# Performance work log

Hardware: AMD Instinct MI355X
Metric: run time of the kernel (lower is better)

Reference implementation:

```python
import jax, jax.numpy as jnp
import numpy as np

NEG_SLOPE = 0.2

def gat_layer(x, W, al, ar, src, dst, n_dst):
    # x: [Ns, Fin]; W: [Fin, H*D]; al/ar: [H, D]; src/dst: [E]
    H, D = al.shape
    h = (x @ W).reshape(-1, H, D)          # [Ns, H, D]
    h_dst = h[:n_dst]                       # dst nodes are prefix of src nodes (DGL block)
    el = (h * al).sum(-1)                   # [Ns, H]
    er = (h_dst * ar).sum(-1)               # [Nd, H]
    e = jax.nn.leaky_relu(el[src] + er[dst], NEG_SLOPE)  # [E, H]
    m = jax.ops.segment_max(e, dst, num_segments=n_dst)  # stable edge-softmax
    a = jnp.exp(e - m[dst])
    s = jax.ops.segment_sum(a, dst, num_segments=n_dst)
    alpha = a / s[dst]                      # [E, H]
    msg = h[src] * alpha[:, :, None]        # [E, H, D]
    out = jax.ops.segment_sum(msg, dst, num_segments=n_dst)  # [Nd, H, D]
    return out.reshape(n_dst, H * D)


def setup_inputs() -> dict:
    key = jax.random.key(0)
    ks = jax.random.split(key, 16)
    N0, N1, N2, N3 = 200000, 100000, 50000, 25000
    E0, E1, E2 = 1000000, 500000, 250000
    Fin, Dh, H, C = 256, 64, 3, 40
    inp = {}
    inp['x'] = jax.random.normal(ks[0], (N0, Fin), jnp.float32)
    inp['src0'] = jax.random.randint(ks[1], (E0,), 0, N0, jnp.int32)
    inp['dst0'] = jnp.sort(jax.random.randint(ks[2], (E0,), 0, N1, jnp.int32))
    inp['src1'] = jax.random.randint(ks[3], (E1,), 0, N1, jnp.int32)
    inp['dst1'] = jnp.sort(jax.random.randint(ks[4], (E1,), 0, N2, jnp.int32))
    inp['src2'] = jax.random.randint(ks[5], (E2,), 0, N2, jnp.int32)
    inp['dst2'] = jnp.sort(jax.random.randint(ks[6], (E2,), 0, N3, jnp.int32))
    sc = lambda f: np.float32(1.0 / np.sqrt(f))
    inp['W0'] = jax.random.normal(ks[7], (Fin, H * Dh), jnp.float32) * sc(Fin)
    inp['al0'] = jax.random.normal(ks[8], (H, Dh), jnp.float32) * sc(Dh)
    inp['ar0'] = jax.random.normal(ks[9], (H, Dh), jnp.float32) * sc(Dh)
    inp['W1'] = jax.random.normal(ks[10], (H * Dh, H * Dh), jnp.float32) * sc(H * Dh)
    inp['al1'] = jax.random.normal(ks[11], (H, Dh), jnp.float32) * sc(Dh)
    inp['ar1'] = jax.random.normal(ks[12], (H, Dh), jnp.float32) * sc(Dh)
    inp['W2'] = jax.random.normal(ks[13], (H * Dh, C), jnp.float32) * sc(H * Dh)
    inp['al2'] = jax.random.normal(ks[14], (1, C), jnp.float32) * sc(C)
    inp['ar2'] = jax.random.normal(ks[15], (1, C), jnp.float32) * sc(C)
    return inp


def reference(x, src0, dst0, src1, dst1, src2, dst2,
              W0, al0, ar0, W1, al1, ar1, W2, al2, ar2):
    N1, N2, N3 = 100000, 50000, 25000
    h = gat_layer(x, W0, al0, ar0, src0, dst0, N1)
    h = jax.nn.relu(h)  # dropout is identity in eval/deterministic mode
    h = gat_layer(h, W1, al1, ar1, src1, dst1, N2)
    h = jax.nn.relu(h)
    out = gat_layer(h, W2, al2, ar2, src2, dst2, N3)  # [N3, n_classes]
    return out
```

## Files before the change

kernel.cpp:

```cpp
#include <hip/hip_runtime.h>
#include <math.h>

#define DEV_INLINE __device__ __forceinline__

typedef __attribute__((ext_vector_type(8))) short short8v;
typedef __attribute__((ext_vector_type(4))) float float4v;

DEV_INLINE unsigned short f2bf_rtn(float f) {
  unsigned u = __float_as_uint(f);
  u += 0x7FFFu + ((u >> 16) & 1u);
  return (unsigned short)(u >> 16);
}
DEV_INLINE float bf2f(unsigned short s) { return __uint_as_float(((unsigned)s) << 16); }

DEV_INLINE int soff(int row, int oct) { return row * 32 + ((oct ^ ((row >> 1) & 3)) << 3); }

DEV_INLINE void gload_lds16(const void* g, void* l) {
  __builtin_amdgcn_global_load_lds(
      (const __attribute__((address_space(1))) void*)g,
      (__attribute__((address_space(3))) void*)l, 16, 0, 0);
}

__global__ void prepass_all(const float* __restrict__ W0, const float* __restrict__ W1,
                            const float* __restrict__ W2, short* __restrict__ w0h,
                            short* __restrict__ w0l, short* __restrict__ w1h,
                            short* __restrict__ w1l, short* __restrict__ w2h,
                            short* __restrict__ w2l,
                            const int* __restrict__ d0, const int* __restrict__ d1,
                            const int* __restrict__ d2, int* __restrict__ o0,
                            int* __restrict__ o1, int* __restrict__ o2,
                            int E0, int E1, int E2, int n1, int n2, int n3) {
  const int S0 = 256 * 192, S1 = 192 * 192, S2 = 192 * 48;
  const int WTOT = S0 + S1 + S2;
  int gidx = blockIdx.x * 256 + threadIdx.x;
  if (gidx < WTOT) {
    int idx = gidx;
    const float* W; short *Wh, *Wl; int K; int which;
    if (idx < S0) { W = W0; Wh = w0h; Wl = w0l; K = 256; which = 0; }
    else if (idx < S0 + S1) { idx -= S0; W = W1; Wh = w1h; Wl = w1l; K = 192; which = 1; }
    else { idx -= S0 + S1; W = W2; Wh = w2h; Wl = w2l; K = 192; which = 2; }
    int n = idx / K, k = idx - n * K;
    if (which == 2 && n >= 40) { Wh[idx] = 0; Wl[idx] = 0; return; }
    int N = (which == 2) ? 40 : 192;
    float w = W[(size_t)k * N + n];
    unsigned short h = f2bf_rtn(w);
    Wh[idx] = (short)h;
    Wl[idx] = (short)f2bf_rtn(w - bf2f(h));
    return;
  }
  int i = gidx - WTOT;
  const int* dst; int* off; int E, nd;
  if (i < E0) { dst = d0; off = o0; E = E0; nd = n1; }
  else if (i < E0 + E1) { i -= E0; dst = d1; off = o1; E = E1; nd = n2; }
  else if (i < E0 + E1 + E2) { i -= E0 + E1; dst = d2; off = o2; E = E2; nd = n3; }
  else return;
  int d = dst[i];
  int p = (i == 0) ? -1 : dst[i - 1];
  for (int q = p + 1; q <= d; ++q) off[q] = i;
  if (i == E - 1)
    for (int q = d + 1; q <= nd; ++q) off[q] = E;
}

#define DMA_B(ktv, bufv)                                                      \
  {                                                                           \
    const int kb = (ktv) << 6;                                \
    for (int c = w; c < NT; c += 4) {                                         \
      gload_lds16((const char*)Bth + (size_t)c * (K * 32) + voff + kb,        \
                  (short*)Bs_h[bufv] + c * 512);                              \
      gload_lds16((const char*)Btl + (size_t)c * (K * 32) + voff + kb,        \
                  (short*)Bs_l[bufv] + c * 512);                              \
    }                                                                         \
  }

template <int NT, int H>
__global__ __launch_bounds__(256, 3) void gemm_fused(
    const float* __restrict__ A, const short* __restrict__ Bth,
    const short* __restrict__ Btl, const float* __restrict__ al,
    const float* __restrict__ ar, float* __restrict__ C,
    float* __restrict__ el, float* __restrict__ er,
    int M, int N, int K, int n_dst) {
  constexpr int BN = NT * 16;
  constexpr int TPH = NT / H;
  __shared__ short Bs_h[2][BN * 32], Bs_l[2][BN * 32];
  const int tid = threadIdx.x;
  const int w = tid >> 6, lane = tid & 63;
  const int quad = lane >> 4, l16 = lane & 15;
  const int m0 = blockIdx.x * 64;
  const int arow = m0 + w * 16 + l16;

  const int voff = (lane >> 2) * (K * 2) + ((((lane & 3) ^ ((lane >> 3) & 3))) << 4);

  float4v acc[NT];
#pragma unroll
  for (int nt = 0; nt < NT; ++nt)
#pragma unroll
    for (int r = 0; r < 4; ++r) acc[nt][r] = 0.f;

  const int nk = K >> 5;

  DMA_B(0, 0);
  float4 pa0, pa1;
  if (arow < M) {
    const float* ap = A + (size_t)arow * K + quad * 8;
    pa0 = *(const float4*)ap;
    pa1 = *(const float4*)(ap + 4);
  } else {
    pa0 = make_float4(0.f, 0.f, 0.f, 0.f);
    pa1 = pa0;
  }
  __syncthreads();

  for (int kt = 0; kt < nk; ++kt) {
    const int cur = kt & 1;
    float4 na0, na1;
    if (kt + 1 < nk) {
      if (arow < M) {
        const float* ap = A + (size_t)arow * K + ((kt + 1) << 5) + quad * 8;
        na0 = *(const float4*)ap;
        na1 = *(const float4*)(ap + 4);
      } else {
        na0 = make_float4(0.f, 0.f, 0.f, 0.f);
        na1 = na0;
      }
      DMA_B(kt + 1, cur ^ 1);
    } else {
      na0 = make_float4(0.f, 0.f, 0.f, 0.f);
      na1 = na0;
    }
    short8v afh, afl;
    {
      float vs[8] = {pa0.x, pa0.y, pa0.z, pa0.w, pa1.x, pa1.y, pa1.z, pa1.w};
#pragma unroll
      for (int j = 0; j < 8; ++j) {
        unsigned short hh = f2bf_rtn(vs[j]);
        afh[j] = (short)hh;
        afl[j] = (short)f2bf_rtn(vs[j] - bf2f(hh));
      }
    }
#pragma unroll
    for (int nt = 0; nt < NT; ++nt) {
      int col = nt * 16 + l16;
      short8v bfh = *(const short8v*)(Bs_h[cur] + soff(col, quad));
      short8v bfl = *(const short8v*)(Bs_l[cur] + soff(col, quad));
      acc[nt] = __builtin_amdgcn_mfma_f32_16x16x32_bf16(afh, bfh, acc[nt], 0, 0, 0);
      acc[nt] = __builtin_amdgcn_mfma_f32_16x16x32_bf16(afh, bfl, acc[nt], 0, 0, 0);
      acc[nt] = __builtin_amdgcn_mfma_f32_16x16x32_bf16(afl, bfh, acc[nt], 0, 0, 0);
    }
    if (kt + 1 < nk) __syncthreads();
    pa0 = na0;
    pa1 = na1;
  }

  float av[NT], rv[NT];
#pragma unroll
  for (int nt = 0; nt < NT; ++nt) {
    int col = nt * 16 + l16;
    av[nt] = (col < N) ? al[col] : 0.f;
    rv[nt] = (col < N) ? ar[col] : 0.f;
  }
#pragma unroll
  for (int r = 0; r < 4; ++r) {
    int gm = m0 + w * 16 + quad * 4 + r;
    if (gm >= M) continue;
    float pl[H], pr[H];
#pragma unroll
    for (int h = 0; h < H; ++h) { pl[h] = 0.f; pr[h] = 0.f; }
#pragma unroll
    for (int nt = 0; nt < NT; ++nt) {
      int h = nt / TPH;
      pl[h] = fmaf(acc[nt][r], av[nt], pl[h]);
      pr[h] = fmaf(acc[nt][r], rv[nt], pr[h]);
    }
#pragma unroll
    for (int h = 0; h < H; ++h) {
#pragma unroll
      for (int o = 8; o >= 1; o >>= 1) {
        pl[h] += __shfl_xor(pl[h], o, 16);
        pr[h] += __shfl_xor(pr[h], o, 16);
      }
    }
    if (l16 == 0) {
#pragma unroll
      for (int h = 0; h < H; ++h) {
        el[gm * H + h] = pl[h];
        if (gm < n_dst) er[gm * H + h] = pr[h];
      }
    }
#pragma unroll
    for (int nt = 0; nt < NT; ++nt) {
      int col = nt * 16 + l16;
      if (col < N) C[(size_t)gm * N + col] = acc[nt][r];
    }
  }
}

template <int H, int D, bool RELU>
__global__ __launch_bounds__(256) void agg2_kernel(
    const float* __restrict__ hsrc, const float* __restrict__ el,
    const float* __restrict__ er, const int* __restrict__ src,
    const int* __restrict__ off, float* __restrict__ out, int n_dst) {
  constexpr int F = H * D;
  constexpr int NP = (F + 63) / 64;
  __shared__ float wbuf[16][16][H];
  __shared__ int sbuf[16][16];
  const int g = threadIdx.x >> 4, l = threadIdx.x & 15;
  const int d = blockIdx.x * 16 + g;
  if (d >= n_dst) return;
  const int lo = off[d], hi = off[d + 1];

  if (hi <= lo) {
#pragma unroll
    for (int p = 0; p < NP; ++p) {
      int c4 = (p * 16 + l) * 4;
      if (c4 < F) *(float4*)(out + (size_t)d * F + c4) = make_float4(0.f, 0.f, 0.f, 0.f);
    }
    return;
  }

  float erv[H], s_part[H];
#pragma unroll
  for (int h = 0; h < H; ++h) {
    erv[h] = er[d * H + h];
    s_part[h] = 0.f;
  }
  float4 acc[NP];
#pragma unroll
  for (int p = 0; p < NP; ++p) acc[p] = make_float4(0.f, 0.f, 0.f, 0.f);

  for (int base = lo; base < hi; base += 16) {
    const int i = base + l;
    const bool valid = i < hi;
    const int sid = valid ? src[i] : 0;
#pragma unroll
    for (int h = 0; h < H; ++h) {
      float e = 0.f;
      if (valid) {
        e = el[sid * H + h] + erv[h];
        e = e > 0.f ? e : 0.2f * e;
        e = __expf(e);
      }
      s_part[h] += e;
      wbuf[g][l][h] = e;
    }
    sbuf[g][l] = sid;

    const int cnt = min(16, hi - base);
    float4 hv[NP], hn[NP], hn2[NP];
    {
      int sj = sbuf[g][0];
#pragma unroll
      for (int p = 0; p < NP; ++p) {
        int c4 = (p * 16 + l) * 4;
        hv[p] = (c4 < F) ? *(const float4*)(hsrc + (size_t)sj * F + c4)
                         : make_float4(0.f, 0.f, 0.f, 0.f);
      }
    }
    if (cnt > 1) {
      int sj = sbuf[g][1];
#pragma unroll
      for (int p = 0; p < NP; ++p) {
        int c4 = (p * 16 + l) * 4;
        hn[p] = (c4 < F) ? *(const float4*)(hsrc + (size_t)sj * F + c4)
                         : make_float4(0.f, 0.f, 0.f, 0.f);
      }
    }
    for (int ei = 0; ei < cnt; ++ei) {
      if (ei + 2 < cnt) {
        int sj2 = sbuf[g][ei + 2];
#pragma unroll
        for (int p = 0; p < NP; ++p) {
          int c4 = (p * 16 + l) * 4;
          hn2[p] = (c4 < F) ? *(const float4*)(hsrc + (size_t)sj2 * F + c4)
                            : make_float4(0.f, 0.f, 0.f, 0.f);
        }
      }
#pragma unroll
      for (int p = 0; p < NP; ++p) {
        int c4 = (p * 16 + l) * 4;
        float wc = wbuf[g][ei][c4 / D];
        acc[p].x = fmaf(wc, hv[p].x, acc[p].x);
        acc[p].y = fmaf(wc, hv[p].y, acc[p].y);
        acc[p].z = fmaf(wc, hv[p].z, acc[p].z);
        acc[p].w = fmaf(wc, hv[p].w, acc[p].w);
      }
#pragma unroll
      for (int p = 0; p < NP; ++p) { hv[p] = hn[p]; hn[p] = hn2[p]; }
    }
  }

#pragma unroll
  for (int h = 0; h < H; ++h)
#pragma unroll
    for (int o = 8; o >= 1; o >>= 1) s_part[h] += __shfl_xor(s_part[h], o, 16);

#pragma unroll
  for (int p = 0; p < NP; ++p) {
    int c4 = (p * 16 + l) * 4;
    if (c4 < F) {
      float inv = 1.f / s_part[c4 / D];
      float4 o;
      o.x = acc[p].x * inv; o.y = acc[p].y * inv;
      o.z = acc[p].z * inv; o.w = acc[p].w * inv;
      if (RELU) {
        o.x = fmaxf(o.x, 0.f); o.y = fmaxf(o.y, 0.f);
        o.z = fmaxf(o.z, 0.f); o.w = fmaxf(o.w, 0.f);
      }
      *(float4*)(out + (size_t)d * F + c4) = o;
    }
  }
}

extern "C" void kernel_launch(void* const* d_in, const int* in_sizes, int n_in,
                              void* d_out, int out_size, void* d_ws, size_t ws_size,
                              hipStream_t stream) {
  const float* x   = (const float*)d_in[0];
  const int* src0  = (const int*)d_in[1];
  const int* dst0  = (const int*)d_in[2];
  const int* src1  = (const int*)d_in[3];
  const int* dst1  = (const int*)d_in[4];
  const int* src2  = (const int*)d_in[5];
  const int* dst2  = (const int*)d_in[6];
  const float* W0  = (const float*)d_in[7];
  const float* al0 = (const float*)d_in[8];
  const float* ar0 = (const float*)d_in[9];
  const float* W1  = (const float*)d_in[10];
  const float* al1 = (const float*)d_in[11];
  const float* ar1 = (const float*)d_in[12];
  const float* W2  = (const float*)d_in[13];
  const float* al2 = (const float*)d_in[14];
  const float* ar2 = (const float*)d_in[15];

  const int N0 = 200000, N1 = 100000, N2 = 50000, N3 = 25000;
  const int E0 = in_sizes[1], E1 = in_sizes[3], E2 = in_sizes[5];
  const int Fin = 256, F = 192, C = 40;

  float* ws     = (float*)d_ws;
  float* h_buf  = ws;
  float* o_buf  = h_buf + (size_t)N0 * F;
  float* el_buf = o_buf + (size_t)N1 * F;
  float* er_buf = el_buf + (size_t)N0 * 3;
  short* w0h    = (short*)(er_buf + (size_t)N1 * 3);
  short* w0l    = w0h + 192 * 256;
  short* w1h    = w0l + 192 * 256;
  short* w1l    = w1h + 192 * 192;
  short* w2h    = w1l + 192 * 192;
  short* w2l    = w2h + 48 * 192;
  int*   off0   = (int*)(w2l + 48 * 192);
  int*   off1   = off0 + (N1 + 1);
  int*   off2   = off1 + (N2 + 1);

  dim3 blk(256);

  const int WTOT = 256 * 192 + 192 * 192 + 192 * 48;
  const int ETOT = E0 + E1 + E2;
  prepass_all<<<dim3((WTOT + ETOT + 255) / 256), blk, 0, stream>>>(
      W0, W1, W2, w0h, w0l, w1h, w1l, w2h, w2l,
      dst0, dst1, dst2, off0, off1, off2, E0, E1, E2, N1, N2, N3);

  gemm_fused<12, 3><<<dim3((N0 + 63) / 64), blk, 0, stream>>>(
      x, w0h, w0l, al0, ar0, h_buf, el_buf, er_buf, N0, F, Fin, N1);
  agg2_kernel<3, 64, true><<<dim3((N1 + 15) / 16), blk, 0, stream>>>(
      h_buf, el_buf, er_buf, src0, off0, o_buf, N1);

  gemm_fused<12, 3><<<dim3((N1 + 63) / 64), blk, 0, stream>>>(
      o_buf, w1h, w1l, al1, ar1, h_buf, el_buf, er_buf, N1, F, F, N2);
  agg2_kernel<3, 64, true><<<dim3((N2 + 15) / 16), blk, 0, stream>>>(
      h_buf, el_buf, er_buf, src1, off1, o_buf, N2);

  gemm_fused<3, 1><<<dim3((N2 + 63) / 64), blk, 0, stream>>>(
      o_buf, w2h, w2l, al2, ar2, h_buf, el_buf, er_buf, N2, C, F, N3);
  agg2_kernel<1, 40, false><<<dim3((N3 + 15) / 16), blk, 0, stream>>>(
      h_buf, el_buf, er_buf, src2, off2, (float*)d_out, N3);
}
```

Before: 641.6 us.

## Double GEMM row tile per wave to reuse B fragments and hand-tune waits

```diff
diff --git a/kernel.cpp b/kernel.cpp
--- a/kernel.cpp
+++ b/kernel.cpp
@@ -73,7 +73,7 @@
   }
 
 template <int NT, int H>
-__global__ __launch_bounds__(256, 3) void gemm_fused(
+__global__ __launch_bounds__(256) void gemm_fused(
     const float* __restrict__ A, const short* __restrict__ Bth,
     const short* __restrict__ Btl, const float* __restrict__ al,
     const float* __restrict__ ar, float* __restrict__ C,
@@ -85,56 +85,61 @@
   const int tid = threadIdx.x;
   const int w = tid >> 6, lane = tid & 63;
   const int quad = lane >> 4, l16 = lane & 15;
-  const int m0 = blockIdx.x * 64;
-  const int arow = m0 + w * 16 + l16;
+  const int m0 = blockIdx.x * 128;
 
   const int voff = (lane >> 2) * (K * 2) + ((((lane & 3) ^ ((lane >> 3) & 3))) << 4);
 
-  float4v acc[NT];
-#pragma unroll
-  for (int nt = 0; nt < NT; ++nt)
-#pragma unroll
-    for (int r = 0; r < 4; ++r) acc[nt][r] = 0.f;
+  const int r0 = min(m0 + w * 32 + l16, M - 1);
+  const int r1 = min(m0 + w * 32 + 16 + l16, M - 1);
+  const float* a0p = A + (size_t)r0 * K + quad * 8;
+  const float* a1p = A + (size_t)r1 * K + quad * 8;
+
+  float4v acc[2][NT];
+#pragma unroll
+  for (int mt = 0; mt < 2; ++mt)
+#pragma unroll
+    for (int nt = 0; nt < NT; ++nt)
+#pragma unroll
+      for (int r = 0; r < 4; ++r) acc[mt][nt][r] = 0.f;
 
   const int nk = K >> 5;
 
   DMA_B(0, 0);
-  float4 pa0, pa1;
-  if (arow < M) {
-    const float* ap = A + (size_t)arow * K + quad * 8;
-    pa0 = *(const float4*)ap;
-    pa1 = *(const float4*)(ap + 4);
-  } else {
-    pa0 = make_float4(0.f, 0.f, 0.f, 0.f);
-    pa1 = pa0;
-  }
-  __syncthreads();
+  asm volatile("" ::: "memory");
+  float4 pa00 = *(const float4*)a0p;
+  float4 pa01 = *(const float4*)(a0p + 4);
+  float4 pa10 = *(const float4*)a1p;
+  float4 pa11 = *(const float4*)(a1p + 4);
+  asm volatile("s_waitcnt vmcnt(4)" ::: "memory");
+  asm volatile("s_barrier" ::: "memory");
 
   for (int kt = 0; kt < nk; ++kt) {
     const int cur = kt & 1;
-    float4 na0, na1;
+    float4 na00, na01, na10, na11;
     if (kt + 1 < nk) {
-      if (arow < M) {
-        const float* ap = A + (size_t)arow * K + ((kt + 1) << 5) + quad * 8;
-        na0 = *(const float4*)ap;
-        na1 = *(const float4*)(ap + 4);
-      } else {
-        na0 = make_float4(0.f, 0.f, 0.f, 0.f);
-        na1 = na0;
-      }
       DMA_B(kt + 1, cur ^ 1);
+      asm volatile("" ::: "memory");
+      const int ko = (kt + 1) << 5;
+      na00 = *(const float4*)(a0p + ko);
+      na01 = *(const float4*)(a0p + ko + 4);
+      na10 = *(const float4*)(a1p + ko);
+      na11 = *(const float4*)(a1p + ko + 4);
     } else {
-      na0 = make_float4(0.f, 0.f, 0.f, 0.f);
-      na1 = na0;
-    }
-    short8v afh, afl;
+      na00 = make_float4(0.f, 0.f, 0.f, 0.f);
+      na01 = na00; na10 = na00; na11 = na00;
+    }
+    short8v afh[2], afl[2];
     {
-      float vs[8] = {pa0.x, pa0.y, pa0.z, pa0.w, pa1.x, pa1.y, pa1.z, pa1.w};
+      float vs0[8] = {pa00.x, pa00.y, pa00.z, pa00.w, pa01.x, pa01.y, pa01.z, pa01.w};
+      float vs1[8] = {pa10.x, pa10.y, pa10.z, pa10.w, pa11.x, pa11.y, pa11.z, pa11.w};
 #pragma unroll
       for (int j = 0; j < 8; ++j) {
-        unsigned short hh = f2bf_rtn(vs[j]);
-        afh[j] = (short)hh;
-        afl[j] = (short)f2bf_rtn(vs[j] - bf2f(hh));
+        unsigned short h0 = f2bf_rtn(vs0[j]);
+        afh[0][j] = (short)h0;
+        afl[0][j] = (short)f2bf_rtn(vs0[j] - bf2f(h0));
+        unsigned short h1 = f2bf_rtn(vs1[j]);
+        afh[1][j] = (short)h1;
+        afl[1][j] = (short)f2bf_rtn(vs1[j] - bf2f(h1));
       }
     }
 #pragma unroll
@@ -142,13 +147,19 @@
       int col = nt * 16 + l16;
       short8v bfh = *(const short8v*)(Bs_h[cur] + soff(col, quad));
       short8v bfl = *(const short8v*)(Bs_l[cur] + soff(col, quad));
-      acc[nt] = __builtin_amdgcn_mfma_f32_16x16x32_bf16(afh, bfh, acc[nt], 0, 0, 0);
-      acc[nt] = __builtin_amdgcn_mfma_f32_16x16x32_bf16(afh, bfl, acc[nt], 0, 0, 0);
-      acc[nt] = __builtin_amdgcn_mfma_f32_16x16x32_bf16(afl, bfh, acc[nt], 0, 0, 0);
-    }
-    if (kt + 1 < nk) __syncthreads();
-    pa0 = na0;
-    pa1 = na1;
+#pragma unroll
+      for (int mt = 0; mt < 2; ++mt) {
+        acc[mt][nt] = __builtin_amdgcn_mfma_f32_16x16x32_bf16(afh[mt], bfh, acc[mt][nt], 0, 0, 0);
+        acc[mt][nt] = __builtin_amdgcn_mfma_f32_16x16x32_bf16(afh[mt], bfl, acc[mt][nt], 0, 0, 0);
+        acc[mt][nt] = __builtin_amdgcn_mfma_f32_16x16x32_bf16(afl[mt], bfh, acc[mt][nt], 0, 0, 0);
+      }
+    }
+    if (kt + 1 < nk) {
+      asm volatile("s_waitcnt lgkmcnt(0)" ::: "memory");
+      asm volatile("s_waitcnt vmcnt(4)" ::: "memory");
+      asm volatile("s_barrier" ::: "memory");
+    }
+    pa00 = na00; pa01 = na01; pa10 = na10; pa11 = na11;
   }
 
   float av[NT], rv[NT];
@@ -159,39 +170,41 @@
     rv[nt] = (col < N) ? ar[col] : 0.f;
   }
 #pragma unroll
-  for (int r = 0; r < 4; ++r) {
-    int gm = m0 + w * 16 + quad * 4 + r;
-    if (gm >= M) continue;
-    float pl[H], pr[H];
-#pragma unroll
-    for (int h = 0; h < H; ++h) { pl[h] = 0.f; pr[h] = 0.f; }
-#pragma unroll
-    for (int nt = 0; nt < NT; ++nt) {
-      int h = nt / TPH;
-      pl[h] = fmaf(acc[nt][r], av[nt], pl[h]);
-      pr[h] = fmaf(acc[nt][r], rv[nt], pr[h]);
-    }
-#pragma unroll
-    for (int h = 0; h < H; ++h) {
-#pragma unroll
-      for (int o = 8; o >= 1; o >>= 1) {
-        pl[h] += __shfl_xor(pl[h], o, 16);
-        pr[h] += __shfl_xor(pr[h], o, 16);
-      }
-    }
-    if (l16 == 0) {
+  for (int mt = 0; mt < 2; ++mt)
+#pragma unroll
+    for (int r = 0; r < 4; ++r) {
+      int gm = m0 + w * 32 + mt * 16 + quad * 4 + r;
+      if (gm >= M) continue;
+      float pl[H], pr[H];
+#pragma unroll
+      for (int h = 0; h < H; ++h) { pl[h] = 0.f; pr[h] = 0.f; }
+#pragma unroll
+      for (int nt = 0; nt < NT; ++nt) {
+        int h = nt / TPH;
+        pl[h] = fmaf(acc[mt][nt][r], av[nt], pl[h]);
+        pr[h] = fmaf(acc[mt][nt][r], rv[nt], pr[h]);
+      }
 #pragma unroll
       for (int h = 0; h < H; ++h) {
-        el[gm * H + h] = pl[h];
-        if (gm < n_dst) er[gm * H + h] = pr[h];
-      }
-    }
-#pragma unroll
-    for (int nt = 0; nt < NT; ++nt) {
-      int col = nt * 16 + l16;
-      if (col < N) C[(size_t)gm * N + col] = acc[nt][r];
-    }
-  }
+#pragma unroll
+        for (int o = 8; o >= 1; o >>= 1) {
+          pl[h] += __shfl_xor(pl[h], o, 16);
+          pr[h] += __shfl_xor(pr[h], o, 16);
+        }
+      }
+      if (l16 == 0) {
+#pragma unroll
+        for (int h = 0; h < H; ++h) {
+          el[gm * H + h] = pl[h];
+          if (gm < n_dst) er[gm * H + h] = pr[h];
+        }
+      }
+#pragma unroll
+      for (int nt = 0; nt < NT; ++nt) {
+        int col = nt * 16 + l16;
+        if (col < N) C[(size_t)gm * N + col] = acc[mt][nt][r];
+      }
+    }
 }
 
 template <int H, int D, bool RELU>
@@ -357,17 +370,17 @@
       W0, W1, W2, w0h, w0l, w1h, w1l, w2h, w2l,
       dst0, dst1, dst2, off0, off1, off2, E0, E1, E2, N1, N2, N3);
 
-  gemm_fused<12, 3><<<dim3((N0 + 63) / 64), blk, 0, stream>>>(
+  gemm_fused<12, 3><<<dim3((N0 + 127) / 128), blk, 0, stream>>>(
       x, w0h, w0l, al0, ar0, h_buf, el_buf, er_buf, N0, F, Fin, N1);
   agg2_kernel<3, 64, true><<<dim3((N1 + 15) / 16), blk, 0, stream>>>(
       h_buf, el_buf, er_buf, src0, off0, o_buf, N1);
 
-  gemm_fused<12, 3><<<dim3((N1 + 63) / 64), blk, 0, stream>>>(
+  gemm_fused<12, 3><<<dim3((N1 + 127) / 128), blk, 0, stream>>>(
       o_buf, w1h, w1l, al1, ar1, h_buf, el_buf, er_buf, N1, F, F, N2);
   agg2_kernel<3, 64, true><<<dim3((N2 + 15) / 16), blk, 0, stream>>>(
       h_buf, el_buf, er_buf, src1, off1, o_buf, N2);
 
-  gemm_fused<3, 1><<<dim3((N2 + 63) / 64), blk, 0, stream>>>(
+  gemm_fused<3, 1><<<dim3((N2 + 127) / 128), blk, 0, stream>>>(
       o_buf, w2h, w2l, al2, ar2, h_buf, el_buf, er_buf, N2, C, F, N3);
   agg2_kernel<1, 40, false><<<dim3((N3 + 15) / 16), blk, 0, stream>>>(
       h_buf, el_buf, er_buf, src2, off2, (float*)d_out, N3);
```

Result: no change. 644.5 us (+0.5%).
